# Kernel optimization log

Measured on AMD Instinct MI355X. Metric: run time of the kernel, lower is better.

## Reference

```python
import jax, jax.numpy as jnp
import numpy as np

B, S, H = 2, 4096, 2048
NUM_HEADS = 32
HEAD_DIM = H // NUM_HEADS  # 64
SCALE = 1.0 / (HEAD_DIM ** 0.5)
D2 = H // 2  # complex rotation dim per the module (full hidden, not per-head)


def setup_inputs() -> dict:
    key = jax.random.key(0)
    ks = jax.random.split(key, 6)
    hidden_states = jax.random.normal(ks[0], (B, S, H), dtype=jnp.float32)
    init = 0.02  # keep logits in a sane range like trained weights
    wq = jax.random.normal(ks[1], (H, H), dtype=jnp.float32) * init
    wk = jax.random.normal(ks[2], (H, H), dtype=jnp.float32) * init
    wv = jax.random.normal(ks[3], (H, H), dtype=jnp.float32) * init
    wo = jax.random.normal(ks[4], (H, H), dtype=jnp.float32) * init
    # standard RoPE frequency table over the D2 complex lanes
    inv_freq = 1.0 / (10000.0 ** (jnp.arange(D2, dtype=jnp.float32) / D2))
    angles = jnp.arange(S, dtype=jnp.float32)[:, None] * inv_freq[None, :]  # [S, D2]
    freqs_cos = jnp.cos(angles)
    freqs_sin = jnp.sin(angles)
    position_ids = jnp.arange(S, dtype=jnp.int64)
    return {
        "hidden_states": hidden_states,
        "wq": wq, "wk": wk, "wv": wv, "wo": wo,
        "freqs_cos": freqs_cos, "freqs_sin": freqs_sin,
        "position_ids": position_ids,
    }


def _rope(x, cos, sin):
    # x: [B, S, H]; complex pair split at H//2 (module-level, not per-head)
    xr, xi = x[..., :D2], x[..., D2:]
    out_r = xr * cos - xi * sin
    out_i = xr * sin + xi * cos
    # torch.view_as_real(...).flatten(2) interleaves (re, im) pairs
    return jnp.stack([out_r, out_i], axis=-1).reshape(x.shape)


def reference(hidden_states, wq, wk, wv, wo, freqs_cos, freqs_sin, position_ids):
    q = jnp.einsum('bsh,oh->bso', hidden_states, wq)
    k = jnp.einsum('bsh,oh->bso', hidden_states, wk)
    v = jnp.einsum('bsh,oh->bso', hidden_states, wv)
    cos = freqs_cos[position_ids]  # [S, D2]
    sin = freqs_sin[position_ids]
    q_rot = _rope(q, cos, sin)
    k_rot = _rope(k, cos, sin)
    scores = jnp.einsum('bqd,bkd->bqk', q_rot, k_rot) * SCALE  # [B, S, S]
    probs = jax.nn.softmax(scores, axis=-1)
    ctx = jnp.einsum('bqk,bkd->bqd', probs, v)
    output = jnp.einsum('bsh,oh->bso', ctx, wo)
    return output, k_rot, v
```

## Files before the change

### kernel.cpp

```cpp
#include <hip/hip_runtime.h>
#include <cstdint>
#include <cstddef>

#define B_    2
#define S_    4096
#define H_    2048
#define D2_   1024
#define SCALE_ 0.125f

typedef __attribute__((ext_vector_type(8))) _Float16 half8;
typedef __attribute__((ext_vector_type(4))) float f32x4;

__device__ __forceinline__ ushort f2h(float f) {
    _Float16 h = (_Float16)f;
    return *(ushort*)&h;
}
__device__ __forceinline__ float h2f(ushort u) {
    return (float)(*(_Float16*)&u);
}

__device__ __forceinline__ void gld_lds16(const ushort* g, ushort* l) {
    __builtin_amdgcn_global_load_lds((const __attribute__((address_space(1))) void*)g,
                                     (__attribute__((address_space(3))) void*)l,
                                     16, 0, 0);
}

__global__ __launch_bounds__(256) void cast_f16_kernel(const float* __restrict__ src,
                                                       ushort* __restrict__ dst, int n4) {
    int i = blockIdx.x * 256 + threadIdx.x;
    if (i < n4) {
        float4 v = ((const float4*)src)[i];
        ushort4 o;
        o.x = f2h(v.x); o.y = f2h(v.y); o.z = f2h(v.z); o.w = f2h(v.w);
        ((ushort4*)dst)[i] = o;
    }
}

__global__ __launch_bounds__(256) void cast4_f16_kernel(const float* __restrict__ w0,
                                                        const float* __restrict__ w1,
                                                        const float* __restrict__ w2,
                                                        const float* __restrict__ w3,
                                                        ushort* __restrict__ o0,
                                                        ushort* __restrict__ o1,
                                                        ushort* __restrict__ o2,
                                                        ushort* __restrict__ o3,
                                                        int n4) {
    int i = blockIdx.x * 256 + threadIdx.x;
    if (i >= n4) return;
    const float* s; ushort* d;
    switch (blockIdx.y) {
        case 0: s = w0; d = o0; break;
        case 1: s = w1; d = o1; break;
        case 2: s = w2; d = o2; break;
        default: s = w3; d = o3; break;
    }
    float4 v = ((const float4*)s)[i];
    ushort4 o;
    o.x = f2h(v.x); o.y = f2h(v.y); o.z = f2h(v.z); o.w = f2h(v.w);
    ((ushort4*)d)[i] = o;
}

#define WAIT_VM(N) asm volatile("s_waitcnt vmcnt(" #N ")" ::: "memory")
#define WAIT_LGKM  asm volatile("s_waitcnt lgkmcnt(0)" ::: "memory")
#define BAR        __builtin_amdgcn_s_barrier()

template <int QM>
__device__ __forceinline__ void ld_a(const ushort* pA, int aRow0, int kx0, int kx1,
                                     half8 (&af)[4][2]) {
#pragma unroll
    for (int mi = 0; mi < 4; mi++) {
        af[mi][0] = *(const half8*)(pA + aRow0 + QM * 4096 + mi * 1024 + kx0);
        af[mi][1] = *(const half8*)(pA + aRow0 + QM * 4096 + mi * 1024 + kx1);
    }
}
template <int QN>
__device__ __forceinline__ void ld_b(const ushort* pB, int bRow0, int kx0, int kx1,
                                     half8 (&bf)[2][2][2]) {
#pragma unroll
    for (int ni = 0; ni < 2; ni++) {
        bf[QN][ni][0] = *(const half8*)(pB + bRow0 + QN * 2048 + ni * 1024 + kx0);
        bf[QN][ni][1] = *(const half8*)(pB + bRow0 + QN * 2048 + ni * 1024 + kx1);
    }
}
template <int QM, int QN>
__device__ __forceinline__ void mma(half8 (&af)[4][2], half8 (&bf)[2][2][2],
                                    f32x4 (&acc)[8][4]) {
    __builtin_amdgcn_s_setprio(1);
#pragma unroll
    for (int mi = 0; mi < 4; mi++)
#pragma unroll
        for (int ni = 0; ni < 2; ni++) {
            acc[QM * 4 + mi][QN * 2 + ni] = __builtin_amdgcn_mfma_f32_16x16x32_f16(
                af[mi][0], bf[QN][ni][0], acc[QM * 4 + mi][QN * 2 + ni], 0, 0, 0);
            acc[QM * 4 + mi][QN * 2 + ni] = __builtin_amdgcn_mfma_f32_16x16x32_f16(
                af[mi][1], bf[QN][ni][1], acc[QM * 4 + mi][QN * 2 + ni], 0, 0, 0);
        }
    __builtin_amdgcn_s_setprio(0);
}

#define TILE(T_, STA_, STB_, VMC_)                                      \
    {                                                                   \
        const int bo_ = ((T_) & 1) << 14;                               \
        ld_a<0>(pAs + bo_, aRow0, kx0, kx1, af);                        \
        ld_b<0>(pBs + bo_, bRow0, kx0, kx1, bf);                        \
        if (STA_) stA((T_) + 1, 0);                                     \
        BAR; WAIT_LGKM;                                                 \
        mma<0, 0>(af, bf, acc);                                         \
        BAR;                                                            \
        ld_b<1>(pBs + bo_, bRow0, kx0, kx1, bf);                        \
        if (STA_) stA((T_) + 1, 1);                                     \
        BAR; WAIT_LGKM;                                                 \
        mma<0, 1>(af, bf, acc);                                         \
        BAR;                                                            \
        ld_a<1>(pAs + bo_, aRow0, kx0, kx1, af);                        \
        if (STB_) stB((T_) + 2, 0);                                     \
        BAR; WAIT_LGKM;                                                 \
        mma<1, 0>(af, bf, acc);                                         \
        BAR;                                                            \
        if (STB_) stB((T_) + 2, 1);                                     \
        VMC_;                                                           \
        BAR;                                                            \
        mma<1, 1>(af, bf, acc);                                         \
        BAR;                                                            \
    }

template <bool HALF_OUT>
__global__ __launch_bounds__(512, 2) void gemm256(const ushort* __restrict__ A,
                                                  const ushort* __restrict__ B,
                                                  void* __restrict__ Cv,
                                                  int M, int N, int K, float alpha,
                                                  size_t sA, size_t sB, size_t sC) {
    __shared__ __align__(16) ushort As[2][256][64];
    __shared__ __align__(16) ushort Bs[2][256][64];

    A += (size_t)blockIdx.z * sA;
    B += (size_t)blockIdx.z * sB;

    const int nwg  = gridDim.x * gridDim.y;
    const int orig = blockIdx.y * gridDim.x + blockIdx.x;
    const int wg   = (orig & 7) * (nwg >> 3) + (orig >> 3);
    const int bm   = (wg / gridDim.x) * 256;
    const int bn   = (wg % gridDim.x) * 256;

    const int tid  = threadIdx.x;
    const int lane = tid & 63;
    const int wave = tid >> 6;
    const int wr   = wave >> 2;
    const int wc   = wave & 3;
    const int col  = lane & 15;
    const int quad = lane >> 4;

    const int srow = tid >> 3;
    const int scol = ((tid & 7) ^ (srow & 7)) * 8;
    const ushort* gA = A + (size_t)(bm + srow) * K + scol;
    const ushort* gB = B + (size_t)(bn + srow) * K + scol;
    const size_t rs64  = (size_t)64 * K;
    const size_t rs128 = (size_t)128 * K;
    ushort* lA = &As[0][0][0] + tid * 8;
    ushort* lB = &Bs[0][0][0] + tid * 8;

    auto stA = [&](int t, int h) {
        const ushort* s = gA + (size_t)t * 64 + (h ? rs128 : (size_t)0);
        ushort* d = lA + ((t & 1) << 14) + (h << 13);
        gld_lds16(s, d);
        gld_lds16(s + rs64, d + 4096);
    };
    auto stB = [&](int t, int h) {
        const ushort* s = gB + (size_t)t * 64 + (h ? rs128 : (size_t)0);
        ushort* d = lB + ((t & 1) << 14) + (h << 13);
        gld_lds16(s, d);
        gld_lds16(s + rs64, d + 4096);
    };

    const int kx0   = ((quad ^ (col & 7)) * 8);
    const int kx1   = (((4 + quad) ^ (col & 7)) * 8);
    const int aRow0 = (wr * 128 + col) * 64;
    const int bRow0 = (wc * 64 + col) * 64;
    const ushort* pAs = &As[0][0][0];
    const ushort* pBs = &Bs[0][0][0];

    f32x4 acc[8][4];
#pragma unroll
    for (int i = 0; i < 8; i++)
#pragma unroll
        for (int j = 0; j < 4; j++) { f32x4 z = {0.f, 0.f, 0.f, 0.f}; acc[i][j] = z; }

    half8 af[4][2];
    half8 bf[2][2][2];

    const int T = K >> 6;

    stB(0, 0); stB(0, 1); stA(0, 0); stA(0, 1); stB(1, 0); stB(1, 1);
    WAIT_VM(4);
    BAR;

    int t = 0;
    for (; t < T - 2; ++t) TILE(t, 1, 1, WAIT_VM(4));
    TILE(t, 1, 0, WAIT_VM(0));
    ++t;
    TILE(t, 0, 0, (void)0);

    ushort* Ch = (ushort*)Cv + (size_t)blockIdx.z * sC;
    float*  Cf = (float*)Cv + (size_t)blockIdx.z * sC;
#pragma unroll
    for (int qm = 0; qm < 2; qm++)
#pragma unroll
        for (int mi = 0; mi < 4; mi++)
#pragma unroll
            for (int qn = 0; qn < 2; qn++)
#pragma unroll
                for (int ni = 0; ni < 2; ni++)
#pragma unroll
                    for (int r = 0; r < 4; r++) {
                        int grow = bm + wr * 128 + qm * 64 + mi * 16 + quad * 4 + r;
                        int gcol = bn + wc * 64 + qn * 32 + ni * 16 + col;
                        float val = alpha * acc[qm * 4 + mi][qn * 2 + ni][r];
                        if (HALF_OUT)
                            Ch[(size_t)grow * N + gcol] = f2h(val);
                        else
                            Cf[(size_t)grow * N + gcol] = val;
                    }
}

__global__ __launch_bounds__(256) void rope_kernel(const ushort* __restrict__ qh,
                                                   const ushort* __restrict__ kh,
                                                   const float* __restrict__ cosT,
                                                   const float* __restrict__ sinT,
                                                   const int* __restrict__ pos,
                                                   ushort* __restrict__ qr,
                                                   ushort* __restrict__ kr,
                                                   float* __restrict__ krf32) {
    int idx = blockIdx.x * 256 + threadIdx.x;
    int row = idx >> 8;
    int jj  = (idx & 255) * 4;
    int p = pos[row & (S_ - 1)];
    const ushort* q = qh + (size_t)row * H_ + jj;
    const ushort* k = kh + (size_t)row * H_ + jj;
    const float* cr = cosT + (size_t)p * D2_ + jj;
    const float* sr = sinT + (size_t)p * D2_ + jj;
    float4 c = *(const float4*)cr;
    float4 sn = *(const float4*)sr;
    ushort4 qr4 = *(const ushort4*)q;
    ushort4 qi4 = *(const ushort4*)(q + D2_);
    ushort4 kr4 = *(const ushort4*)k;
    ushort4 ki4 = *(const ushort4*)(k + D2_);

    float qrv[4] = {h2f(qr4.x), h2f(qr4.y), h2f(qr4.z), h2f(qr4.w)};
    float qiv[4] = {h2f(qi4.x), h2f(qi4.y), h2f(qi4.z), h2f(qi4.w)};
    float krv[4] = {h2f(kr4.x), h2f(kr4.y), h2f(kr4.z), h2f(kr4.w)};
    float kiv[4] = {h2f(ki4.x), h2f(ki4.y), h2f(ki4.z), h2f(ki4.w)};
    float cv[4] = {c.x, c.y, c.z, c.w};
    float sv[4] = {sn.x, sn.y, sn.z, sn.w};

    ushort qo[8], ko[8];
    float kf[8];
#pragma unroll
    for (int t = 0; t < 4; t++) {
        float o0 = qrv[t] * cv[t] - qiv[t] * sv[t];
        float o1 = qrv[t] * sv[t] + qiv[t] * cv[t];
        qo[2 * t] = f2h(o0); qo[2 * t + 1] = f2h(o1);
        float p0 = krv[t] * cv[t] - kiv[t] * sv[t];
        float p1 = krv[t] * sv[t] + kiv[t] * cv[t];
        ko[2 * t] = f2h(p0); ko[2 * t + 1] = f2h(p1);
        kf[2 * t] = p0; kf[2 * t + 1] = p1;
    }
    ushort* qro = qr + (size_t)row * H_ + 2 * jj;
    ushort* kro = kr + (size_t)row * H_ + 2 * jj;
    float* krf  = krf32 + (size_t)row * H_ + 2 * jj;
    *(ushort4*)(qro)     = *(ushort4*)(qo);
    *(ushort4*)(qro + 4) = *(ushort4*)(qo + 4);
    *(ushort4*)(kro)     = *(ushort4*)(ko);
    *(ushort4*)(kro + 4) = *(ushort4*)(ko + 4);
    *(float4*)(krf)      = *(float4*)(kf);
    *(float4*)(krf + 4)  = *(float4*)(kf + 4);
}

__global__ __launch_bounds__(256) void transpose_cast_kernel(const float* __restrict__ v,
                                                             ushort* __restrict__ vt) {
    __shared__ float tile[32][33];
    int b  = blockIdx.z;
    int s0 = blockIdx.y * 32, h0 = blockIdx.x * 32;
    const float* vb = v + (size_t)b * S_ * H_;
    ushort* vtb = vt + (size_t)b * H_ * S_;
    int tx = threadIdx.x & 31, ty = threadIdx.x >> 5;
#pragma unroll
    for (int i = 0; i < 32; i += 8)
        tile[ty + i][tx] = vb[(size_t)(s0 + ty + i) * H_ + h0 + tx];
    __syncthreads();
#pragma unroll
    for (int i = 0; i < 32; i += 8)
        vtb[(size_t)(h0 + ty + i) * S_ + s0 + tx] = f2h(tile[tx][ty + i]);
}

__global__ __launch_bounds__(256) void softmax_kernel(const float* __restrict__ sc,
                                                      ushort* __restrict__ pr) {
    __shared__ float red[8];
    size_t row = blockIdx.x;
    const float4* r = (const float4*)(sc + row * (size_t)S_);
    int tid = threadIdx.x;
    float4 v[4];
    float m = -1e30f;
#pragma unroll
    for (int i = 0; i < 4; i++) {
        v[i] = r[tid + i * 256];
        m = fmaxf(m, fmaxf(fmaxf(v[i].x, v[i].y), fmaxf(v[i].z, v[i].w)));
    }
#pragma unroll
    for (int off = 32; off >= 1; off >>= 1) m = fmaxf(m, __shfl_xor(m, off));
    if ((tid & 63) == 0) red[tid >> 6] = m;
    __syncthreads();
    m = fmaxf(fmaxf(red[0], red[1]), fmaxf(red[2], red[3]));
    float s = 0.f;
#pragma unroll
    for (int i = 0; i < 4; i++) {
        v[i].x = __expf(v[i].x - m); v[i].y = __expf(v[i].y - m);
        v[i].z = __expf(v[i].z - m); v[i].w = __expf(v[i].w - m);
        s += v[i].x + v[i].y + v[i].z + v[i].w;
    }
#pragma unroll
    for (int off = 32; off >= 1; off >>= 1) s += __shfl_xor(s, off);
    if ((tid & 63) == 0) red[4 + (tid >> 6)] = s;
    __syncthreads();
    float inv = 1.0f / (red[4] + red[5] + red[6] + red[7]);
    ushort4* o = (ushort4*)(pr + row * (size_t)S_);
#pragma unroll
    for (int i = 0; i < 4; i++) {
        ushort4 u;
        u.x = f2h(v[i].x * inv); u.y = f2h(v[i].y * inv);
        u.z = f2h(v[i].z * inv); u.w = f2h(v[i].w * inv);
        o[tid + i * 256] = u;
    }
}

extern "C" void kernel_launch(void* const* d_in, const int* in_sizes, int n_in,
                              void* d_out, int out_size, void* d_ws, size_t ws_size,
                              hipStream_t stream) {
    const float* hs   = (const float*)d_in[0];
    const float* wq   = (const float*)d_in[1];
    const float* wk   = (const float*)d_in[2];
    const float* wv   = (const float*)d_in[3];
    const float* wo   = (const float*)d_in[4];
    const float* fcos = (const float*)d_in[5];
    const float* fsin = (const float*)d_in[6];
    const int*   pos  = (const int*)d_in[7];

    const size_t BSH = (size_t)B_ * S_ * H_;
    const size_t HH  = (size_t)H_ * H_;

    float* out      = (float*)d_out;
    float* krot_out = out + BSH;
    float* v_out    = krot_out + BSH;

    char* ws = (char*)d_ws;
    const size_t MB = 1ull << 20;
    ushort* Xb  = (ushort*)(ws + 0);
    ushort* Wqb = (ushort*)(ws + 32 * MB);
    ushort* Wkb = (ushort*)(ws + 40 * MB);
    ushort* Wvb = (ushort*)(ws + 48 * MB);
    ushort* Wob = (ushort*)(ws + 56 * MB);
    ushort* qh  = (ushort*)(ws + 64 * MB);
    ushort* kh  = (ushort*)(ws + 96 * MB);
    ushort* qrb = (ushort*)(ws + 128 * MB);
    ushort* krb = (ushort*)(ws + 160 * MB);
    ushort* vtb = (ushort*)(ws + 192 * MB);
    float*  sc  = (float*)(ws + 224 * MB);
    ushort* prb = (ushort*)(ws + 64 * MB);
    ushort* cb  = (ushort*)(ws + 128 * MB);

    cast_f16_kernel<<<(int)(BSH / 4 / 256), 256, 0, stream>>>(hs, Xb, (int)(BSH / 4));
    cast4_f16_kernel<<<dim3((int)(HH / 4 / 256), 4), 256, 0, stream>>>(
        wq, wk, wv, wo, Wqb, Wkb, Wvb, Wob, (int)(HH / 4));

    dim3 gProj(H_ / 256, (B_ * S_) / 256, 1);
    gemm256<true ><<<gProj, 512, 0, stream>>>(Xb, Wqb, qh,    B_ * S_, H_, H_, 1.0f, 0, 0, 0);
    gemm256<true ><<<gProj, 512, 0, stream>>>(Xb, Wkb, kh,    B_ * S_, H_, H_, 1.0f, 0, 0, 0);
    gemm256<false><<<gProj, 512, 0, stream>>>(Xb, Wvb, v_out, B_ * S_, H_, H_, 1.0f, 0, 0, 0);

    rope_kernel<<<(B_ * S_ * (D2_ / 4)) / 256, 256, 0, stream>>>(
        qh, kh, fcos, fsin, pos, qrb, krb, krot_out);

    transpose_cast_kernel<<<dim3(H_ / 32, S_ / 32, B_), 256, 0, stream>>>(v_out, vtb);

    dim3 gSc(S_ / 256, S_ / 256, B_);
    gemm256<false><<<gSc, 512, 0, stream>>>(qrb, krb, sc, S_, S_, H_, SCALE_,
                                            (size_t)S_ * H_, (size_t)S_ * H_,
                                            (size_t)S_ * S_);

    softmax_kernel<<<B_ * S_, 256, 0, stream>>>(sc, prb);

    dim3 gPV(H_ / 256, S_ / 256, B_);
    gemm256<true><<<gPV, 512, 0, stream>>>(prb, vtb, cb, S_, H_, S_, 1.0f,
                                           (size_t)S_ * S_, (size_t)H_ * S_,
                                           (size_t)S_ * H_);

    gemm256<false><<<gProj, 512, 0, stream>>>(cb, Wob, out, B_ * S_, H_, H_, 1.0f, 0, 0, 0);
}
```

Measured before the change: 0.9997 ms.

## Restructure GEMM main loop into double-buffered register-prefetch pipeline

Replaces the four-phase TILE macro, which had barriers and LDS waits around each MFMA quarter and prefetched B two tiles ahead, with a simpler loop. Each iteration issues all global-to-LDS loads for the next tile, then runs the four MFMA quarters using separate A/B register fragments. It finishes with one full vmcnt wait, one barrier, and a prefetch of the next tile's first fragments. The intent is to cut barrier count and let the compiler overlap LDS reads with MFMAs. The cost is a shallower global prefetch, which waits for all outstanding loads every tile. Launch bounds drop to one block per CU, which allows more registers but lowers occupancy.

```diff
diff --git a/kernel.cpp b/kernel.cpp
--- a/kernel.cpp
+++ b/kernel.cpp
@@ -61,7 +61,6 @@
 }
 
 #define WAIT_VM(N) asm volatile("s_waitcnt vmcnt(" #N ")" ::: "memory")
-#define WAIT_LGKM  asm volatile("s_waitcnt lgkmcnt(0)" ::: "memory")
 #define BAR        __builtin_amdgcn_s_barrier()
 
 template <int QM>
@@ -75,57 +74,31 @@
 }
 template <int QN>
 __device__ __forceinline__ void ld_b(const ushort* pB, int bRow0, int kx0, int kx1,
-                                     half8 (&bf)[2][2][2]) {
+                                     half8 (&bf)[2][2]) {
 #pragma unroll
     for (int ni = 0; ni < 2; ni++) {
-        bf[QN][ni][0] = *(const half8*)(pB + bRow0 + QN * 2048 + ni * 1024 + kx0);
-        bf[QN][ni][1] = *(const half8*)(pB + bRow0 + QN * 2048 + ni * 1024 + kx1);
+        bf[ni][0] = *(const half8*)(pB + bRow0 + QN * 2048 + ni * 1024 + kx0);
+        bf[ni][1] = *(const half8*)(pB + bRow0 + QN * 2048 + ni * 1024 + kx1);
     }
 }
 template <int QM, int QN>
-__device__ __forceinline__ void mma(half8 (&af)[4][2], half8 (&bf)[2][2][2],
+__device__ __forceinline__ void mma(const half8 (&af)[4][2], const half8 (&bf)[2][2],
                                     f32x4 (&acc)[8][4]) {
     __builtin_amdgcn_s_setprio(1);
 #pragma unroll
     for (int mi = 0; mi < 4; mi++)
 #pragma unroll
         for (int ni = 0; ni < 2; ni++) {
-            acc[QM * 4 + mi][QN * 2 + ni] = __builtin_amdgcn_mfma_f32_16x16x32_f16(
-                af[mi][0], bf[QN][ni][0], acc[QM * 4 + mi][QN * 2 + ni], 0, 0, 0);
-            acc[QM * 4 + mi][QN * 2 + ni] = __builtin_amdgcn_mfma_f32_16x16x32_f16(
-                af[mi][1], bf[QN][ni][1], acc[QM * 4 + mi][QN * 2 + ni], 0, 0, 0);
+            f32x4 c = acc[QM * 4 + mi][QN * 2 + ni];
+            c = __builtin_amdgcn_mfma_f32_16x16x32_f16(af[mi][0], bf[ni][0], c, 0, 0, 0);
+            c = __builtin_amdgcn_mfma_f32_16x16x32_f16(af[mi][1], bf[ni][1], c, 0, 0, 0);
+            acc[QM * 4 + mi][QN * 2 + ni] = c;
         }
     __builtin_amdgcn_s_setprio(0);
 }
 
-#define TILE(T_, STA_, STB_, VMC_)                                      \
-    {                                                                   \
-        const int bo_ = ((T_) & 1) << 14;                               \
-        ld_a<0>(pAs + bo_, aRow0, kx0, kx1, af);                        \
-        ld_b<0>(pBs + bo_, bRow0, kx0, kx1, bf);                        \
-        if (STA_) stA((T_) + 1, 0);                                     \
-        BAR; WAIT_LGKM;                                                 \
-        mma<0, 0>(af, bf, acc);                                         \
-        BAR;                                                            \
-        ld_b<1>(pBs + bo_, bRow0, kx0, kx1, bf);                        \
-        if (STA_) stA((T_) + 1, 1);                                     \
-        BAR; WAIT_LGKM;                                                 \
-        mma<0, 1>(af, bf, acc);                                         \
-        BAR;                                                            \
-        ld_a<1>(pAs + bo_, aRow0, kx0, kx1, af);                        \
-        if (STB_) stB((T_) + 2, 0);                                     \
-        BAR; WAIT_LGKM;                                                 \
-        mma<1, 0>(af, bf, acc);                                         \
-        BAR;                                                            \
-        if (STB_) stB((T_) + 2, 1);                                     \
-        VMC_;                                                           \
-        BAR;                                                            \
-        mma<1, 1>(af, bf, acc);                                         \
-        BAR;                                                            \
-    }
-
 template <bool HALF_OUT>
-__global__ __launch_bounds__(512, 2) void gemm256(const ushort* __restrict__ A,
+__global__ __launch_bounds__(512, 1) void gemm256(const ushort* __restrict__ A,
                                                   const ushort* __restrict__ B,
                                                   void* __restrict__ Cv,
                                                   int M, int N, int K, float alpha,
@@ -185,20 +158,35 @@
 #pragma unroll
         for (int j = 0; j < 4; j++) { f32x4 z = {0.f, 0.f, 0.f, 0.f}; acc[i][j] = z; }
 
-    half8 af[4][2];
-    half8 bf[2][2][2];
+    half8 af0[4][2], af1[4][2], bf0[2][2], bf1[2][2];
 
     const int T = K >> 6;
 
-    stB(0, 0); stB(0, 1); stA(0, 0); stA(0, 1); stB(1, 0); stB(1, 1);
-    WAIT_VM(4);
+    stA(0, 0); stA(0, 1); stB(0, 0); stB(0, 1);
+    WAIT_VM(0);
     BAR;
-
-    int t = 0;
-    for (; t < T - 2; ++t) TILE(t, 1, 1, WAIT_VM(4));
-    TILE(t, 1, 0, WAIT_VM(0));
-    ++t;
-    TILE(t, 0, 0, (void)0);
+    ld_a<0>(pAs, aRow0, kx0, kx1, af0);
+    ld_b<0>(pBs, bRow0, kx0, kx1, bf0);
+
+    for (int t = 0; t < T; ++t) {
+        const int bo = (t & 1) << 14;
+        if (t + 1 < T) {
+            stA(t + 1, 0); stA(t + 1, 1); stB(t + 1, 0); stB(t + 1, 1);
+        }
+        ld_a<1>(pAs + bo, aRow0, kx0, kx1, af1);
+        mma<0, 0>(af0, bf0, acc);
+        mma<1, 0>(af1, bf0, acc);
+        ld_b<1>(pBs + bo, bRow0, kx0, kx1, bf1);
+        mma<0, 1>(af0, bf1, acc);
+        mma<1, 1>(af1, bf1, acc);
+        if (t + 1 < T) {
+            WAIT_VM(0);
+            BAR;
+            const int bo2 = ((t + 1) & 1) << 14;
+            ld_a<0>(pAs + bo2, aRow0, kx0, kx1, af0);
+            ld_b<0>(pBs + bo2, bRow0, kx0, kx1, bf0);
+        }
+    }
 
     ushort* Ch = (ushort*)Cv + (size_t)blockIdx.z * sC;
     float*  Cf = (float*)Cv + (size_t)blockIdx.z * sC;
```

Result: no change. 983.0 us (-1.7%).
